# Performance work log

Hardware: AMD Instinct MI355X
Metric: run time of the kernel (lower is better)

Reference implementation:

```python
import jax, jax.numpy as jnp
import numpy as np
import math

N, D = 4096, 1024


def setup_inputs() -> dict:
    key = jax.random.key(0)
    ks = jax.random.split(key, 8)
    vecs = jax.random.normal(ks[0], (N, D), dtype=jnp.float32)
    mass = jax.random.uniform(ks[1], (N,), dtype=jnp.float32)            # semantic mass in [0,1)
    hops = jax.random.uniform(ks[2], (N,), dtype=jnp.float32) * 5.0      # hop distances in [0,5)
    alive = jax.random.randint(ks[3], (N,), 0, 10) > 0
    is_photon = jax.random.randint(ks[4], (N,), 0, 10) == 0
    W_res_w = jax.random.normal(ks[5], (D, D), dtype=jnp.float32) / np.sqrt(D)
    W_res_b = jnp.zeros((D,), dtype=jnp.float32)
    w_conf_i = jax.random.normal(ks[6], (D,), dtype=jnp.float32) / np.sqrt(2 * D)
    w_conf_j = jax.random.normal(ks[7], (D,), dtype=jnp.float32) / np.sqrt(2 * D)
    b_conf = jnp.zeros((), dtype=jnp.float32)
    log_c = jnp.asarray(math.log(50.0), dtype=jnp.float32)  # 'relationship' domain
    log_G = jnp.zeros((), dtype=jnp.float32)
    return dict(vecs=vecs, mass=mass, hops=hops, alive=alive, is_photon=is_photon,
                W_res_w=W_res_w, W_res_b=W_res_b, w_conf_i=w_conf_i, w_conf_j=w_conf_j,
                b_conf=b_conf, log_c=log_c, log_G=log_G)


def reference(vecs, mass, hops, alive, is_photon, W_res_w, W_res_b,
              w_conf_i, w_conf_j, b_conf, log_c, log_G):
    n = vecs.shape[0]
    c = jnp.maximum(jnp.exp(log_c), 1e-6)
    G = jnp.exp(log_G)

    # Per-row quantities (phi() reads hops/photon from entity i).
    d_light = hops / c                                                   # [N]
    lam = jnp.where(is_photon, 1.0, jnp.exp(-d_light))                   # redshift, [N]
    r2 = jnp.maximum(d_light, 0.1) ** 2                                  # r_safe^2, [N]
    causal_decay = jnp.where(d_light <= 1.0, 1.0, jnp.exp(-d_light + 1.0))  # [N]

    # Causal mask: j must be strictly in the past (j < i).
    idx = jnp.arange(n)
    past = (idx[None, :] < idx[:, None]).astype(vecs.dtype)              # [N,N]
    C = past * causal_decay[:, None]

    # Gravity: G * m_i * m_j / r_i^2
    grav = G * (mass / r2)[:, None] * mass[None, :]                      # [N,N]

    # Resonance: cosine similarity of W_res projections (torch eps=1e-8 norm clamp).
    v = vecs @ W_res_w.T + W_res_b                                       # [N,D]
    vn = v / jnp.maximum(jnp.linalg.norm(v, axis=-1, keepdims=True), 1e-8)
    R = vn @ vn.T                                                        # [N,N]
    zero_norm = jnp.linalg.norm(vecs, axis=-1) < 1e-8                    # [N]
    R = jnp.where(zero_norm[:, None] | zero_norm[None, :], 0.0, R)

    # Conflict gate: sigmoid(W_conflict @ concat(v_i, v_j) + b) = sigmoid(s_i + s_j + b).
    s_i = vecs @ w_conf_i                                                # [N]
    s_j = vecs @ w_conf_j                                                # [N]
    conflict = jax.nn.sigmoid(s_i[:, None] + s_j[None, :] + b_conf)      # [N,N]

    phi_attract = lam[:, None] * grav * C * (0.5 + 0.5 * R)
    phi_repulse = -lam[:, None] * conflict * mass[:, None] * mass[None, :]
    phi = jnp.where(conflict > 0.8, phi_repulse, phi_attract)

    # Black holes and the diagonal produce zero field.
    gate = alive[:, None] & alive[None, :]
    phi = jnp.where(gate & (idx[:, None] != idx[None, :]), phi, 0.0)
    return phi
```

## Files before the change

kernel.cpp:

```cpp
#include <hip/hip_runtime.h>
#include <hip/hip_bf16.h>
#include <math.h>

#define NROW 4096
#define DIM  1024

typedef short v8s __attribute__((ext_vector_type(8)));
typedef float v4f __attribute__((ext_vector_type(4)));

#define GLD16(src, dst) __builtin_amdgcn_global_load_lds( \
    (const __attribute__((address_space(1))) void*)(src), \
    (__attribute__((address_space(3))) void*)(dst), 16, 0, 0)

__device__ __forceinline__ ushort f2bf(float f) {
    __hip_bfloat16 h = __float2bfloat16(f);
    union { __hip_bfloat16 h; ushort u; } x; x.h = h; return x.u;
}
__device__ __forceinline__ ushort4 cvt4(float4 a) {
    ushort4 r; r.x = f2bf(a.x); r.y = f2bf(a.y); r.z = f2bf(a.z); r.w = f2bf(a.w);
    return r;
}

__global__ __launch_bounds__(256) void k_stats(
    const float* vecs, const float* __restrict__ mass,
    const float* __restrict__ hops, const int* __restrict__ alive,
    const int* __restrict__ is_photon, const float* __restrict__ wci,
    const float* __restrict__ wcj, const float* __restrict__ logc,
    const float* __restrict__ logG, const float* __restrict__ bconf,
    const float* W,
    ushort* vsh, int vstr, ushort* wsh, int wstr,
    double* __restrict__ s_i, double* __restrict__ s_j,
    float* __restrict__ rowAtt, float* __restrict__ rowRep,
    float* __restrict__ massF, int* __restrict__ flags,
    float* __restrict__ rownorm)
{
    const int t = threadIdx.x;
    const int wid = t >> 6, lane = t & 63;

    if (blockIdx.x >= NROW / 4) {
        const int row = (blockIdx.x - NROW / 4) * 4 + wid;
        const float* wr = W + (size_t)row * DIM;
        ushort4 uc[4];
        #pragma unroll
        for (int q = 0; q < 4; ++q)
            uc[q] = cvt4(*(const float4*)&wr[lane * 4 + q * 256]);
        __syncthreads();
        ushort* wb = wsh + (size_t)row * wstr;
        #pragma unroll
        for (int q = 0; q < 4; ++q)
            *(ushort4*)&wb[lane * 4 + q * 256] = uc[q];
        return;
    }

    const int row = blockIdx.x * 4 + wid;
    const float* vr = vecs + (size_t)row * DIM;
    double di = 0.0, dj = 0.0, ss = 0.0;
    ushort4 uc[4];
    #pragma unroll
    for (int q = 0; q < 4; ++q) {
        int base = lane * 4 + q * 256;
        float4 pv = *(const float4*)&vr[base];
        float4 pi = *(const float4*)&wci[base];
        float4 pj = *(const float4*)&wcj[base];
        di += (double)pv.x * pi.x + (double)pv.y * pi.y + (double)pv.z * pi.z + (double)pv.w * pi.w;
        dj += (double)pv.x * pj.x + (double)pv.y * pj.y + (double)pv.z * pj.z + (double)pv.w * pj.w;
        ss += (double)pv.x * pv.x + (double)pv.y * pv.y + (double)pv.z * pv.z + (double)pv.w * pv.w;
        uc[q] = cvt4(pv);
    }
    __syncthreads();
    ushort* vb = vsh + (size_t)row * vstr;
    #pragma unroll
    for (int q = 0; q < 4; ++q)
        *(ushort4*)&vb[lane * 4 + q * 256] = uc[q];
    #pragma unroll
    for (int off = 32; off > 0; off >>= 1) {
        di += __shfl_down(di, off);
        dj += __shfl_down(dj, off);
        ss += __shfl_down(ss, off);
    }
    if (lane == 0) {
        double c  = fmax(exp((double)logc[0]), 1e-6);
        double G  = exp((double)logG[0]);
        double dl = (double)hops[row] / c;
        double lam = (is_photon[row] != 0) ? 1.0 : exp(-dl);
        double rs  = fmax(dl, 0.1);
        double cd  = (dl <= 1.0) ? 1.0 : exp(-dl + 1.0);
        double m   = (double)mass[row];
        s_i[row] = di;
        s_j[row] = dj + (double)bconf[0];
        rowAtt[row] = (float)(lam * G * m / (rs * rs) * cd);
        rowRep[row] = (float)(-lam * m);
        massF[row]  = (float)m;
        flags[row]  = ((alive[row] != 0) ? 1 : 0) | ((sqrt(ss) < 1e-8) ? 2 : 0);
        rownorm[row] = 0.0f;
    }
}

__global__ __launch_bounds__(256) void k_proj(
    const ushort* __restrict__ vsh, int vstr,
    const ushort* __restrict__ wsh, int wstr,
    const float* __restrict__ bias, ushort* __restrict__ vout,
    float* __restrict__ rownorm)
{
    __shared__ ushort As[64 * 64], Bs[64 * 64];
    const int t = threadIdx.x;
    const int m0 = blockIdx.y * 64, n0 = blockIdx.x * 64;
    const int wid = t >> 6, lane = t & 63;
    const int wm = wid >> 1, wn = wid & 1;
    const int quad = lane >> 4, l16 = lane & 15;
    const int sr = t >> 3, sc = t & 7;
    v4f acc[2][2];
    #pragma unroll
    for (int i = 0; i < 2; i++)
        #pragma unroll
        for (int j = 0; j < 2; j++) acc[i][j] = (v4f){0.f, 0.f, 0.f, 0.f};

    #pragma unroll
    for (int p = 0; p < 2; ++p) {
        int r = p * 32 + sr;
        int ksw = (sc ^ (r & 7)) * 8;
        GLD16(&vsh[(size_t)(m0 + r) * vstr + ksw], &As[p * 2048 + wid * 512]);
        GLD16(&wsh[(size_t)(n0 + r) * wstr + ksw], &Bs[p * 2048 + wid * 512]);
    }
    __syncthreads();

    for (int k0 = 0; k0 < DIM; k0 += 64) {
        #pragma unroll
        for (int ks = 0; ks < 2; ++ks) {
            v8s af[2], bfr[2];
            #pragma unroll
            for (int mi = 0; mi < 2; mi++) {
                int row = wm * 32 + mi * 16 + l16;
                af[mi] = *(const v8s*)&As[row * 64 + (((ks * 4 + quad) ^ (l16 & 7)) * 8)];
            }
            #pragma unroll
            for (int ni = 0; ni < 2; ni++) {
                int row = wn * 32 + ni * 16 + l16;
                bfr[ni] = *(const v8s*)&Bs[row * 64 + (((ks * 4 + quad) ^ (l16 & 7)) * 8)];
            }
            #pragma unroll
            for (int mi = 0; mi < 2; mi++)
                #pragma unroll
                for (int ni = 0; ni < 2; ni++)
                    acc[mi][ni] = __builtin_amdgcn_mfma_f32_16x16x32_bf16(af[mi], bfr[ni], acc[mi][ni], 0, 0, 0);
        }
        if (k0 + 64 < DIM) {
            __syncthreads();
            int k1 = k0 + 64;
            #pragma unroll
            for (int p = 0; p < 2; ++p) {
                int r = p * 32 + sr;
                int ksw = (sc ^ (r & 7)) * 8;
                GLD16(&vsh[(size_t)(m0 + r) * vstr + k1 + ksw], &As[p * 2048 + wid * 512]);
                GLD16(&wsh[(size_t)(n0 + r) * wstr + k1 + ksw], &Bs[p * 2048 + wid * 512]);
            }
            __syncthreads();
        }
    }

    float bcol[2];
    #pragma unroll
    for (int ni = 0; ni < 2; ni++) bcol[ni] = bias[n0 + wn * 32 + ni * 16 + l16];
    #pragma unroll
    for (int mi = 0; mi < 2; mi++)
        #pragma unroll
        for (int r = 0; r < 4; r++) {
            int row = m0 + wm * 32 + mi * 16 + quad * 4 + r;
            float ss = 0.0f;
            #pragma unroll
            for (int ni = 0; ni < 2; ni++) {
                int col = n0 + wn * 32 + ni * 16 + l16;
                float vv = acc[mi][ni][r] + bcol[ni];
                vout[(size_t)row * DIM + col] = f2bf(vv);
                ss += vv * vv;
            }
            #pragma unroll
            for (int off = 8; off > 0; off >>= 1) ss += __shfl_down(ss, off);
            if (l16 == 0) atomicAdd(&rownorm[row], ss);
        }
}

__global__ __launch_bounds__(256) void k_phi(
    const ushort* __restrict__ vn,
    const double* __restrict__ s_i, const double* __restrict__ s_j,
    const float* __restrict__ rowAtt, const float* __restrict__ rowRep,
    const float* __restrict__ massF, const int* __restrict__ flags,
    const float* __restrict__ rownorm, float* __restrict__ out)
{
    __shared__ ushort As[64 * 32], Bs[64 * 32];
    const int t = threadIdx.x;
    const int id = blockIdx.x;
    int r = (int)((sqrtf(8.0f * (float)id + 1.0f) - 1.0f) * 0.5f);
    while ((((r + 1) * (r + 2)) >> 1) <= id) ++r;
    while (((r * (r + 1)) >> 1) > id) --r;
    const int bi = r, bj = id - ((r * (r + 1)) >> 1);
    const bool diag = (bi == bj);
    const int m0 = bi * 64, n0 = bj * 64;
    const int wid = t >> 6, lane = t & 63;
    const int wm = wid >> 1, wn = wid & 1;
    const int quad = lane >> 4, l16 = lane & 15;
    const int sr = t >> 2, sc = t & 3;
    const double LN4 = 1.3862943611198906;

    auto ISSUE = [&](int k0) {
        int ksw = (sc ^ ((sr >> 1) & 3)) * 8;
        GLD16(&vn[(size_t)(m0 + sr) * DIM + k0 + ksw], &As[t * 8]);
        GLD16(&vn[(size_t)(n0 + sr) * DIM + k0 + ksw], &Bs[t * 8]);
    };
    ISSUE(0);

    if (!diag) {
        double csjL[2]; float cmL[2]; int colL[2];
        #pragma unroll
        for (int ni = 0; ni < 2; ni++) {
            int col = m0 + wn * 32 + ni * 16 + l16;
            colL[ni] = col;
            csjL[ni] = s_j[col];
            cmL[ni]  = (flags[col] & 1) ? massF[col] : 0.f;
        }
        #pragma unroll
        for (int mi = 0; mi < 2; mi++)
            #pragma unroll
            for (int rr = 0; rr < 4; rr++) {
                int row = n0 + wm * 32 + mi * 16 + quad * 4 + rr;
                double si = s_i[row];
                float  rRm = (flags[row] & 1) ? rowRep[row] : 0.f;
                size_t ob = (size_t)row * NROW;
                #pragma unroll
                for (int ni = 0; ni < 2; ni++) {
                    double x = si + csjL[ni];
                    float v = 0.f;
                    if (x > LN4) {
                        float e = __expf(-(float)x);
                        v = rRm * cmL[ni] * __builtin_amdgcn_rcpf(1.0f + e);
                    }
                    out[ob + colL[ni]] = v;
                }
            }
    }

    double csjH[2]; float cmn[2], cc[2]; int colH[2];
    #pragma unroll
    for (int ni = 0; ni < 2; ni++) {
        int col = n0 + wn * 32 + ni * 16 + l16;
        int cf = flags[col];
        float cma = (cf & 1) ? massF[col] : 0.f;
        colH[ni] = col;
        csjH[ni] = s_j[col];
        cmn[ni]  = cma;
        cc[ni]   = (cf & 2) ? 0.f
                 : cma * __builtin_amdgcn_rcpf(fmaxf(sqrtf(rownorm[col]), 1e-8f));
    }

    v4f acc[2][2];
    #pragma unroll
    for (int i = 0; i < 2; i++)
        #pragma unroll
        for (int j = 0; j < 2; j++) acc[i][j] = (v4f){0.f, 0.f, 0.f, 0.f};

    __syncthreads();
    for (int k0 = 0; k0 < DIM; k0 += 32) {
        v8s af[2], bfr[2];
        #pragma unroll
        for (int mi = 0; mi < 2; mi++) {
            int row = wm * 32 + mi * 16 + l16;
            af[mi] = *(const v8s*)&As[row * 32 + ((quad ^ ((l16 >> 1) & 3)) * 8)];
        }
        #pragma unroll
        for (int ni = 0; ni < 2; ni++) {
            int row = wn * 32 + ni * 16 + l16;
            bfr[ni] = *(const v8s*)&Bs[row * 32 + ((quad ^ ((l16 >> 1) & 3)) * 8)];
        }
        #pragma unroll
        for (int mi = 0; mi < 2; mi++)
            #pragma unroll
            for (int ni = 0; ni < 2; ni++)
                acc[mi][ni] = __builtin_amdgcn_mfma_f32_16x16x32_bf16(af[mi], bfr[ni], acc[mi][ni], 0, 0, 0);
        if (k0 + 32 < DIM) {
            __syncthreads();
            ISSUE(k0 + 32);
            __syncthreads();
        }
    }

    #pragma unroll
    for (int mi = 0; mi < 2; mi++)
        #pragma unroll
        for (int rr = 0; rr < 4; rr++) {
            int row = m0 + wm * 32 + mi * 16 + quad * 4 + rr;
            int fi = flags[row];
            float rA  = rowAtt[row];
            float riv = __builtin_amdgcn_rcpf(fmaxf(sqrtf(rownorm[row]), 1e-8f));
            float a1  = (fi & 1) ? 0.5f * rA : 0.f;
            float a2  = ((fi & 3) == 1) ? 0.5f * rA * riv : 0.f;
            float rRm = (fi & 1) ? rowRep[row] : 0.f;
            double si = s_i[row];
            size_t ob = (size_t)row * NROW;
            #pragma unroll
            for (int ni = 0; ni < 2; ni++) {
                int col = colH[ni];
                double x = si + csjH[ni];
                float  acv = acc[mi][ni][rr];
                float  att = fmaf(a2 * cc[ni], acv, a1 * cmn[ni]);
                float  e   = __expf(-(float)x);
                float  rep = rRm * cmn[ni] * __builtin_amdgcn_rcpf(1.0f + e);
                float  v   = (x > LN4) ? rep : att;
                if (diag) {
                    if (col > row) v = (x > LN4) ? rep : 0.f;
                    if (col == row) v = 0.f;
                }
                out[ob + col] = v;
            }
        }
}

extern "C" void kernel_launch(void* const* d_in, const int* in_sizes, int n_in,
                              void* d_out, int out_size, void* d_ws, size_t ws_size,
                              hipStream_t stream)
{
    const float* vecs      = (const float*)d_in[0];
    const float* mass      = (const float*)d_in[1];
    const float* hops      = (const float*)d_in[2];
    const int*   alive     = (const int*)d_in[3];
    const int*   is_photon = (const int*)d_in[4];
    const float* W         = (const float*)d_in[5];
    const float* Wb        = (const float*)d_in[6];
    const float* wci       = (const float*)d_in[7];
    const float* wcj       = (const float*)d_in[8];
    const float* bconf     = (const float*)d_in[9];
    const float* logc      = (const float*)d_in[10];
    const float* logG      = (const float*)d_in[11];

    char* ws = (char*)d_ws;
    double* s_i     = (double*)(ws);
    double* s_j     = (double*)(ws + 32768);
    float*  rowAtt  = (float*)(ws + 65536);
    float*  rowRep  = (float*)(ws + 81920);
    float*  massF   = (float*)(ws + 98304);
    int*    flagsA  = (int*)(ws + 114688);
    float*  rownorm = (float*)(ws + 131072);
    ushort* vn      = (ushort*)(ws + 147456);

    const size_t VSH_OFF = 147456 + (size_t)NROW * DIM * 2;
    const size_t WSH_OFF = VSH_OFF + (size_t)NROW * DIM * 2;
    const size_t NEED    = WSH_OFF + (size_t)DIM * DIM * 2;
    ushort *vsh, *wsh; int vstr, wstr;
    if (ws_size >= NEED) {
        vsh = (ushort*)(ws + VSH_OFF); vstr = DIM;
        wsh = (ushort*)(ws + WSH_OFF); wstr = DIM;
    } else {
        vsh = (ushort*)vecs + 1024; vstr = 2048;
        wsh = (ushort*)W + 1024;    wstr = 2048;
    }

    k_stats<<<dim3(NROW / 4 + DIM / 4), dim3(256), 0, stream>>>(
        vecs, mass, hops, alive, is_photon, wci, wcj, logc, logG, bconf, W,
        vsh, vstr, wsh, wstr,
        s_i, s_j, rowAtt, rowRep, massF, flagsA, rownorm);
    k_proj<<<dim3(DIM / 64, NROW / 64), dim3(256), 0, stream>>>(
        vsh, vstr, wsh, wstr, Wb, vn, rownorm);
    k_phi<<<dim3(2080), dim3(256), 0, stream>>>(
        vn, s_i, s_j, rowAtt, rowRep, massF, flagsA, rownorm, (float*)d_out);
}
```

Before: 178.0 us.

## Double K-step per LDS stage, remap block order, raise occupancy hint

The phi GEMM now loads 64-wide K tiles into LDS with an 8-way XOR swizzle and runs two MFMA k-substeps per stage. This halves the number of barrier pairs and global-load issue points per tile. Block IDs are permuted in strides of 260 so concurrently running blocks are spread across the triangular tile space, and launch_bounds requests 5 waves-per-EU occupancy. LDS use doubles, which could limit occupancy, and the remap assumes exactly 2080 blocks.

```diff
diff --git a/kernel.cpp b/kernel.cpp
--- a/kernel.cpp
+++ b/kernel.cpp
@@ -180,16 +180,17 @@
         }
 }
 
-__global__ __launch_bounds__(256) void k_phi(
+__global__ __launch_bounds__(256, 5) void k_phi(
     const ushort* __restrict__ vn,
     const double* __restrict__ s_i, const double* __restrict__ s_j,
     const float* __restrict__ rowAtt, const float* __restrict__ rowRep,
     const float* __restrict__ massF, const int* __restrict__ flags,
     const float* __restrict__ rownorm, float* __restrict__ out)
 {
-    __shared__ ushort As[64 * 32], Bs[64 * 32];
+    __shared__ ushort As[64 * 64], Bs[64 * 64];
     const int t = threadIdx.x;
-    const int id = blockIdx.x;
+    const int raw = blockIdx.x;
+    const int id = (raw & 7) * 260 + (raw >> 3);
     int r = (int)((sqrtf(8.0f * (float)id + 1.0f) - 1.0f) * 0.5f);
     while ((((r + 1) * (r + 2)) >> 1) <= id) ++r;
     while (((r * (r + 1)) >> 1) > id) --r;
@@ -199,15 +200,16 @@
     const int wid = t >> 6, lane = t & 63;
     const int wm = wid >> 1, wn = wid & 1;
     const int quad = lane >> 4, l16 = lane & 15;
-    const int sr = t >> 2, sc = t & 3;
+    const int sr = t >> 3, sc = t & 7;
     const double LN4 = 1.3862943611198906;
 
-    auto ISSUE = [&](int k0) {
-        int ksw = (sc ^ ((sr >> 1) & 3)) * 8;
-        GLD16(&vn[(size_t)(m0 + sr) * DIM + k0 + ksw], &As[t * 8]);
-        GLD16(&vn[(size_t)(n0 + sr) * DIM + k0 + ksw], &Bs[t * 8]);
-    };
-    ISSUE(0);
+    #pragma unroll
+    for (int p = 0; p < 2; ++p) {
+        int rr = p * 32 + sr;
+        int ksw = (sc ^ (rr & 7)) * 8;
+        GLD16(&vn[(size_t)(m0 + rr) * DIM + ksw], &As[p * 2048 + wid * 512]);
+        GLD16(&vn[(size_t)(n0 + rr) * DIM + ksw], &Bs[p * 2048 + wid * 512]);
+    }
 
     if (!diag) {
         double csjL[2]; float cmL[2]; int colL[2];
@@ -259,26 +261,36 @@
         for (int j = 0; j < 2; j++) acc[i][j] = (v4f){0.f, 0.f, 0.f, 0.f};
 
     __syncthreads();
-    for (int k0 = 0; k0 < DIM; k0 += 32) {
-        v8s af[2], bfr[2];
-        #pragma unroll
-        for (int mi = 0; mi < 2; mi++) {
-            int row = wm * 32 + mi * 16 + l16;
-            af[mi] = *(const v8s*)&As[row * 32 + ((quad ^ ((l16 >> 1) & 3)) * 8)];
-        }
-        #pragma unroll
-        for (int ni = 0; ni < 2; ni++) {
-            int row = wn * 32 + ni * 16 + l16;
-            bfr[ni] = *(const v8s*)&Bs[row * 32 + ((quad ^ ((l16 >> 1) & 3)) * 8)];
-        }
-        #pragma unroll
-        for (int mi = 0; mi < 2; mi++)
-            #pragma unroll
-            for (int ni = 0; ni < 2; ni++)
-                acc[mi][ni] = __builtin_amdgcn_mfma_f32_16x16x32_bf16(af[mi], bfr[ni], acc[mi][ni], 0, 0, 0);
-        if (k0 + 32 < DIM) {
+    for (int k0 = 0; k0 < DIM; k0 += 64) {
+        #pragma unroll
+        for (int ks = 0; ks < 2; ++ks) {
+            v8s af[2], bfr[2];
+            #pragma unroll
+            for (int mi = 0; mi < 2; mi++) {
+                int row = wm * 32 + mi * 16 + l16;
+                af[mi] = *(const v8s*)&As[row * 64 + (((ks * 4 + quad) ^ (l16 & 7)) * 8)];
+            }
+            #pragma unroll
+            for (int ni = 0; ni < 2; ni++) {
+                int row = wn * 32 + ni * 16 + l16;
+                bfr[ni] = *(const v8s*)&Bs[row * 64 + (((ks * 4 + quad) ^ (l16 & 7)) * 8)];
+            }
+            #pragma unroll
+            for (int mi = 0; mi < 2; mi++)
+                #pragma unroll
+                for (int ni = 0; ni < 2; ni++)
+                    acc[mi][ni] = __builtin_amdgcn_mfma_f32_16x16x32_bf16(af[mi], bfr[ni], acc[mi][ni], 0, 0, 0);
+        }
+        if (k0 + 64 < DIM) {
             __syncthreads();
-            ISSUE(k0 + 32);
+            int k1 = k0 + 64;
+            #pragma unroll
+            for (int p = 0; p < 2; ++p) {
+                int rr = p * 32 + sr;
+                int ksw = (sc ^ (rr & 7)) * 8;
+                GLD16(&vn[(size_t)(m0 + rr) * DIM + k1 + ksw], &As[p * 2048 + wid * 512]);
+                GLD16(&vn[(size_t)(n0 + rr) * DIM + k1 + ksw], &Bs[p * 2048 + wid * 512]);
+            }
             __syncthreads();
         }
     }
@@ -298,7 +310,6 @@
             size_t ob = (size_t)row * NROW;
             #pragma unroll
             for (int ni = 0; ni < 2; ni++) {
-                int col = colH[ni];
                 double x = si + csjH[ni];
                 float  acv = acc[mi][ni][rr];
                 float  att = fmaf(a2 * cc[ni], acv, a1 * cmn[ni]);
@@ -306,10 +317,11 @@
                 float  rep = rRm * cmn[ni] * __builtin_amdgcn_rcpf(1.0f + e);
                 float  v   = (x > LN4) ? rep : att;
                 if (diag) {
+                    int col = colH[ni];
                     if (col > row) v = (x > LN4) ? rep : 0.f;
                     if (col == row) v = 0.f;
                 }
-                out[ob + col] = v;
+                out[ob + colH[ni]] = v;
             }
         }
 }
```

Result: faster. 167.8 us (-5.7%).
